# Optimization experiments

Hardware: AMD Instinct MI355X
Metric: run time of the kernel (lower is better)

## Reference

```python
import jax, jax.numpy as jnp
import numpy as np

H = 32; W = 32; KH = 3; KW = 3; NH = 8; DIM = 256; MLP_DIM = 1024; B = 4; T_FULL = 9
DH = DIM // NH
NEG = -1e9


def layernorm(x, g, b):
    m = jnp.mean(x, axis=-1, keepdims=True)
    v = jnp.var(x, axis=-1, keepdims=True)
    return (x - m) / jnp.sqrt(v + 1e-5) * g + b


def rope(x):
    # x: (B, NH, T, DH); split-half rotary position embedding
    T, dh = x.shape[-2], x.shape[-1]
    inv = 1.0 / (10000.0 ** (jnp.arange(0, dh, 2, dtype=jnp.float32) / dh))
    ang = jnp.arange(T, dtype=jnp.float32)[:, None] * inv  # (T, dh/2)
    cos, sin = jnp.cos(ang), jnp.sin(ang)
    x1, x2 = jnp.split(x, 2, axis=-1)
    return jnp.concatenate([x1 * cos - x2 * sin, x1 * sin + x2 * cos], axis=-1)


def setup_inputs() -> dict:
    key = jax.random.key(0)
    ks = jax.random.split(key, 16)
    def w(i, shp):
        return jax.random.normal(ks[i], shp, jnp.float32) * 0.02
    d = {
        'query': jax.random.normal(ks[0], (B, T_FULL, H * W, DIM), jnp.float32),
        'spatial_mask': jnp.zeros((1,), bool),          # unused by forward (module builds its own)
        'temporal_mask': jnp.zeros((T_FULL, T_FULL), bool),
        'sln_g': jnp.ones((DIM,), jnp.float32), 'sln_b': jnp.zeros((DIM,), jnp.float32),
        's_wq': w(1, (DIM, DIM)), 's_bq': jnp.zeros((DIM,), jnp.float32),
        's_wk': w(2, (DIM, DIM)), 's_bk': jnp.zeros((DIM,), jnp.float32),
        's_wv': w(3, (DIM, DIM)), 's_bv': jnp.zeros((DIM,), jnp.float32),
        's_wo': w(4, (DIM, DIM)), 's_bo': jnp.zeros((DIM,), jnp.float32),
        'tln_g': jnp.ones((DIM,), jnp.float32), 'tln_b': jnp.zeros((DIM,), jnp.float32),
        't_wq': w(5, (DIM, DIM)), 't_bq': jnp.zeros((DIM,), jnp.float32),
        't_wk': w(6, (DIM, DIM)), 't_bk': jnp.zeros((DIM,), jnp.float32),
        't_wv': w(7, (DIM, DIM)), 't_bv': jnp.zeros((DIM,), jnp.float32),
        't_wo': w(8, (DIM, DIM)), 't_bo': jnp.zeros((DIM,), jnp.float32),
        'mln_g': jnp.ones((DIM,), jnp.float32), 'mln_b': jnp.zeros((DIM,), jnp.float32),
        'w1': w(9, (DIM, MLP_DIM)), 'b1': jnp.zeros((MLP_DIM,), jnp.float32),
        'w2': w(10, (MLP_DIM, DIM)), 'b2': jnp.zeros((DIM,), jnp.float32),
    }
    return d


def _forward(query, temporal_mask, sln_g, sln_b, s_wq, s_bq, s_wk, s_bk, s_wv, s_bv, s_wo, s_bo,
             tln_g, tln_b, t_wq, t_bq, t_wk, t_bk, t_wv, t_bv, t_wo, t_bo,
             mln_g, mln_b, w1, b1, w2, b2):
    Bq, Tq, HWn, Dn = query.shape
    T = Tq - 1
    size = KH * KW
    scale = 1.0 / jnp.sqrt(jnp.float32(DH))

    # ---- spatial windowed attention on frames [:-1] (unfold -> per-window 1x9 attention) ----
    visual = query[:, :T].reshape(Bq * T, H, W, Dn)
    pad = jnp.pad(visual, ((0, 0), (KH // 2, KH // 2), (KW // 2, KW // 2), (0, 0)))
    neigh = jnp.stack([pad[:, i:i + H, j:j + W, :] for i in range(KH) for j in range(KW)], axis=1)
    neigh = neigh.reshape(Bq * T, size, HWn, Dn).transpose(0, 2, 1, 3)  # (BT, HW, size, D)
    onep = jnp.pad(jnp.ones((H, W), jnp.float32), ((KH // 2, KH // 2), (KW // 2, KW // 2)))
    valid = jnp.stack([onep[i:i + H, j:j + W] for i in range(KH) for j in range(KW)], axis=0)
    pad_mask = (valid.reshape(size, HWn).T == 0)  # (HW, size) True where neighbor from padding

    vis = visual.reshape(Bq * T, HWn, 1, Dn)
    vis_n = layernorm(vis, sln_g, sln_b)
    nei_n = layernorm(neigh, sln_g, sln_b)
    q = (vis_n @ s_wq + s_bq).reshape(Bq * T, HWn, 1, NH, DH)
    k = (nei_n @ s_wk + s_bk).reshape(Bq * T, HWn, size, NH, DH)
    v = (nei_n @ s_wv + s_bv).reshape(Bq * T, HWn, size, NH, DH)
    scores = jnp.einsum('bnqhd,bnkhd->bnhqk', q, k) * scale
    scores = jnp.where(pad_mask[None, :, None, None, :], NEG, scores)
    attn = jax.nn.softmax(scores, axis=-1)
    o = jnp.einsum('bnhqk,bnkhd->bnqhd', attn, v).reshape(Bq * T, HWn, 1, Dn)
    o = o @ s_wo + s_bo
    x_sp = (o + vis).reshape(Bq, T, HWn, Dn)

    x = jnp.concatenate([x_sp, query[:, -1:]], axis=1)  # (B, T_, HW, D)

    # ---- temporal RoPE attention per spatial location ----
    xt = x.transpose(0, 2, 1, 3).reshape(Bq * HWn, Tq, Dn)
    xn = layernorm(xt, tln_g, tln_b)
    qt = rope((xn @ t_wq + t_bq).reshape(-1, Tq, NH, DH).transpose(0, 2, 1, 3))
    kt = rope((xn @ t_wk + t_bk).reshape(-1, Tq, NH, DH).transpose(0, 2, 1, 3))
    vt = (xn @ t_wv + t_bv).reshape(-1, Tq, NH, DH).transpose(0, 2, 1, 3)
    sc = jnp.einsum('bhqd,bhkd->bhqk', qt, kt) * scale
    sc = jnp.where(temporal_mask[None, None, :, :], NEG, sc)
    at = jax.nn.softmax(sc, axis=-1)
    ot = jnp.einsum('bhqk,bhkd->bhqd', at, vt).transpose(0, 2, 1, 3).reshape(-1, Tq, Dn)
    xt = (ot @ t_wo + t_bo) + xt
    x = xt.reshape(Bq, HWn, Tq, Dn).transpose(0, 2, 1, 3)

    # CLS frame (t=0): average over spatial positions, broadcast back
    avg_cls = jnp.mean(x[:, 0], axis=1, keepdims=True)  # (B, 1, D)
    x = x.at[:, 0].set(jnp.broadcast_to(avg_cls, (Bq, HWn, Dn)))

    # ---- MLP block ----
    xm = layernorm(x, mln_g, mln_b)
    xm = jax.nn.gelu(xm @ w1 + b1, approximate=False) @ w2 + b2
    return xm + x


def reference(query, spatial_mask, temporal_mask, sln_g, sln_b, s_wq, s_bq, s_wk, s_bk, s_wv, s_bv, s_wo, s_bo, tln_g, tln_b, t_wq, t_bq, t_wk, t_bk, t_wv, t_bv, t_wo, t_bo, mln_g, mln_b, w1, b1, w2, b2):
    # spatial_mask is accepted but unused by the original forward (it rebuilds its own)
    return _forward(query, temporal_mask, sln_g, sln_b, s_wq, s_bq, s_wk, s_bk, s_wv, s_bv, s_wo, s_bo,
                    tln_g, tln_b, t_wq, t_bq, t_wk, t_bk, t_wv, t_bv, t_wo, t_bo,
                    mln_g, mln_b, w1, b1, w2, b2)
```

## Files before the change

kernel.cpp:

```cpp
#include <hip/hip_runtime.h>
#include <math.h>

#define TQ_  9

typedef unsigned int   u32;
typedef unsigned short ushort_t;
typedef short bf16x8 __attribute__((ext_vector_type(8)));
typedef float f32x4  __attribute__((ext_vector_type(4)));

__device__ __forceinline__ float bs2f(ushort_t s) {
  return __uint_as_float(((u32)s) << 16);
}
__device__ __forceinline__ ushort_t f2bs(float x) {
  u32 u = __float_as_uint(x);
  u32 r = (u + 0x7FFFu + ((u >> 16) & 1u)) >> 16;
  return (ushort_t)r;
}

__device__ __forceinline__ float gelu_f(float x) {
  float z = x * 0.70710678118654752f;
  float a = fabsf(z);
  float t = __builtin_amdgcn_rcpf(1.f + 0.3275911f * a);
  float poly = t * (0.254829592f + t * (-0.284496736f +
               t * (1.421413741f + t * (-1.453152027f + t * 1.061405429f))));
  float erfv = 1.f - poly * __expf(-z * z);
  erfv = (z < 0.f) ? -erfv : erfv;
  return 0.5f * x * (1.f + erfv);
}

struct TPA { const float* s[10]; ushort_t* d[10]; int K[10]; int N[10]; int pm[10]; };

__global__ __launch_bounds__(256)
void pack_all_kernel(TPA p) {
  int z = blockIdx.z;
  int K = p.K[z], N = p.N[z];
  int bn = blockIdx.x << 5, bk = blockIdx.y << 5;
  if (bn >= N || bk >= K) return;
  const float* W = p.s[z];
  ushort_t* pk = p.d[z];
  int pm = p.pm[z];
  __shared__ float t[32][33];
  int tid = threadIdx.x;
  int tx = tid & 31, ty = tid >> 5;
  #pragma unroll
  for (int r = 0; r < 4; ++r)
    t[ty + (r << 3)][tx] = W[(long)(bk + ty + (r << 3)) * N + bn + tx];
  __syncthreads();
  if (tid < 128) {
    int jl = tid >> 6, q = (tid >> 4) & 3, ln = tid & 15;
    int j = (bn >> 4) + jl, kk = bk >> 5;
    int colsrc = pm ? ((ln & 7) + (jl << 3) + ((ln & 8) << 1))
                    : ((jl << 4) + ln);
    long G = (((long)j * (K >> 5) + kk) << 6) + (q << 4) + ln;
    bf16x8 ov;
    #pragma unroll
    for (int e = 0; e < 8; ++e)
      ov[e] = (short)f2bs(t[(q << 3) + e][colsrc]);
    *(bf16x8*)(pk + (G << 3)) = ov;
  }
}

struct BC6 { const float* b[6]; };
__global__ __launch_bounds__(768)
void bias_concat_kernel(BC6 p, float* __restrict__ dst) {
  int z = blockIdx.x, n = threadIdx.x;
  int w = n >> 8, q = n & 255;
  int psrc = q;
  if (w < 2)
    psrc = (q & 0xE0) | (q & 7) | (((q >> 4) & 1) << 3) | (((q >> 3) & 1) << 4);
  dst[z * 768 + n] = p.b[z * 3 + w][psrc];
}

__global__ __launch_bounds__(256)
void ln_norm_kernel(const float* __restrict__ src, int spatial,
                    const float* __restrict__ g, const float* __restrict__ b,
                    ushort_t* __restrict__ dst) {
  int row = blockIdx.x * 4 + (threadIdx.x >> 6);
  int lane = threadIdx.x & 63;
  long srow = row;
  if (spatial) {
    int bq = row >> 13, r = row & 8191;
    srow = ((long)(bq * TQ_ + (r >> 10)) << 10) + (r & 1023);
  }
  float4 v = ((const float4*)(src + srow * 256))[lane];
  float s  = v.x + v.y + v.z + v.w;
  float s2 = v.x * v.x + v.y * v.y + v.z * v.z + v.w * v.w;
  #pragma unroll
  for (int m = 32; m; m >>= 1) {
    s  += __shfl_xor(s,  m, 64);
    s2 += __shfl_xor(s2, m, 64);
  }
  float mean = s * (1.f / 256.f);
  float rstd = rsqrtf(s2 * (1.f / 256.f) - mean * mean + 1e-5f);
  float4 gv = ((const float4*)g)[lane];
  float4 bv = ((const float4*)b)[lane];
  ushort_t o[4];
  o[0] = f2bs((v.x - mean) * rstd * gv.x + bv.x);
  o[1] = f2bs((v.y - mean) * rstd * gv.y + bv.y);
  o[2] = f2bs((v.z - mean) * rstd * gv.z + bv.z);
  o[3] = f2bs((v.w - mean) * rstd * gv.w + bv.w);
  u32 lo = (u32)o[0] | ((u32)o[1] << 16);
  u32 hi = (u32)o[2] | ((u32)o[3] << 16);
  uint2 pk; pk.x = lo; pk.y = hi;
  *(uint2*)(dst + (long)row * 256 + lane * 4) = pk;
}

template<int K>
__global__ __launch_bounds__(256, 4)
void wgemm_kernel(const ushort_t* __restrict__ A, int lda,
                  const ushort_t* __restrict__ packW,
                  const float* __restrict__ bias, const float* __restrict__ resid,
                  float* __restrict__ Cf, ushort_t* __restrict__ Cb,
                  int N, int NBq, int resid_mode, int out_mode, int act, int rope) {
  constexpr int K32 = K / 32;
  constexpr int AD = (K32 >= 4) ? 4 : K32;
  constexpr int BD = 2;

  int tid = threadIdx.x;
  int wv = tid >> 6, lane = tid & 63;
  int ln = lane & 15, q4 = lane >> 4;

  int gid = blockIdx.x;
  int g = gid >> 5, r = gid & 31;
  int nq = (r >> 3) + ((g % NBq) << 2);
  int mb = ((g / NBq) << 3) + (r & 7);
  int m0 = mb << 7, n0 = nq << 6;

  const ushort_t* Ap = A + (long)(m0 + (wv << 5) + ln) * lda + (q4 << 3);
  long a16 = (long)lda << 4;
  const ushort_t* Bp = packW + (((long)(nq << 2) * K32) << 9) + (lane << 3);

  bf16x8 xr[AD][2];
  bf16x8 wr[BD][4];
  #pragma unroll
  for (int d = 0; d < BD; ++d)
    #pragma unroll
    for (int j = 0; j < 4; ++j)
      wr[d][j] = *(const bf16x8*)(Bp + (((long)j * K32 + d) << 9));
  #pragma unroll
  for (int d = 0; d < AD; ++d) {
    xr[d][0] = *(const bf16x8*)(Ap + d * 32);
    xr[d][1] = *(const bf16x8*)(Ap + a16 + d * 32);
  }

  f32x4 acc[2][4];
  #pragma unroll
  for (int i = 0; i < 2; ++i)
    #pragma unroll
    for (int j = 0; j < 4; ++j) acc[i][j] = 0.f;

  #pragma unroll
  for (int kk = 0; kk < K32; ++kk) {
    #pragma unroll
    for (int i = 0; i < 2; ++i)
      #pragma unroll
      for (int j = 0; j < 4; ++j)
        acc[i][j] = __builtin_amdgcn_mfma_f32_16x16x32_bf16(
            wr[kk % BD][j], xr[kk % AD][i], acc[i][j], 0, 0, 0);
    if (kk + AD < K32) {
      xr[kk % AD][0] = *(const bf16x8*)(Ap + (kk + AD) * 32);
      xr[kk % AD][1] = *(const bf16x8*)(Ap + a16 + (kk + AD) * 32);
    }
    if (kk + BD < K32) {
      #pragma unroll
      for (int j = 0; j < 4; ++j)
        wr[kk % BD][j] = *(const bf16x8*)(Bp + (((long)j * K32 + kk + BD) << 9));
    }
    __builtin_amdgcn_sched_barrier(0);
  }

  float4 bj[4];
  #pragma unroll
  for (int j = 0; j < 4; ++j)
    bj[j] = *(const float4*)(bias + n0 + (j << 4) + (q4 << 2));

  float cs_c[2][4], cs_s[2][4];
  if (rope) {
    int t = (m0 >> 10) % TQ_;
    #pragma unroll
    for (int p = 0; p < 2; ++p)
      #pragma unroll
      for (int r2 = 0; r2 < 4; ++r2) {
        float d = (float)(((q4 & 1) << 2) + r2 + (p << 3));
        float ang = (float)t * exp2f(d * -0.8304820237218406f);
        cs_c[p][r2] = cosf(ang);
        float s = sinf(ang);
        cs_s[p][r2] = (q4 & 2) ? s : -s;
      }
  }

  #pragma unroll
  for (int i = 0; i < 2; ++i) {
    int m = m0 + (wv << 5) + (i << 4) + ln;
    long orow = m;
    if (out_mode == 1 || resid_mode == 2) {
      int bq = m >> 13, rr = m & 8191;
      orow = ((long)(bq * TQ_ + (rr >> 10)) << 10) + (rr & 1023);
    }
    #pragma unroll
    for (int j = 0; j < 4; ++j) {
      int n = n0 + (j << 4) + (q4 << 2);
      float v[4];
      #pragma unroll
      for (int r2 = 0; r2 < 4; ++r2) v[r2] = acc[i][j][r2] + bj[j][r2];
      if (rope && ((nq << 2) + j) < 32) {
        #pragma unroll
        for (int r2 = 0; r2 < 4; ++r2) {
          float other = __shfl_xor(v[r2], 32, 64);
          v[r2] = v[r2] * cs_c[j & 1][r2] + other * cs_s[j & 1][r2];
        }
      }
      if (act) {
        #pragma unroll
        for (int r2 = 0; r2 < 4; ++r2) v[r2] = gelu_f(v[r2]);
      }
      if (resid_mode == 1) {
        float4 rv = *(const float4*)(resid + (long)m * 256 + n);
        v[0] += rv.x; v[1] += rv.y; v[2] += rv.z; v[3] += rv.w;
      } else if (resid_mode == 2) {
        float4 rv = *(const float4*)(resid + orow * 256 + n);
        v[0] += rv.x; v[1] += rv.y; v[2] += rv.z; v[3] += rv.w;
      }
      if (out_mode == 2) {
        uint2 pk;
        pk.x = (u32)f2bs(v[0]) | ((u32)f2bs(v[1]) << 16);
        pk.y = (u32)f2bs(v[2]) | ((u32)f2bs(v[3]) << 16);
        *(uint2*)(Cb + (long)m * N + n) = pk;
      } else {
        float4 o4; o4.x = v[0]; o4.y = v[1]; o4.z = v[2]; o4.w = v[3];
        if (out_mode == 1) *(float4*)(Cf + orow * 256 + n) = o4;
        else               *(float4*)(Cf + (long)m * N + n) = o4;
      }
    }
  }
}

__device__ __forceinline__ int tl_off(int row, int col) {
  return (row << 8) + (((((col >> 3) + row) & 31)) << 3) + (col & 7);
}

__global__ __launch_bounds__(512, 6)
void mlp_fused_kernel(float* xio,
                      const ushort_t* __restrict__ W1p,
                      const float* __restrict__ b1,
                      const ushort_t* __restrict__ W2p,
                      const float* __restrict__ b2,
                      const float* __restrict__ g,
                      const float* __restrict__ be) {
  __shared__ ushort_t XL[8192];
  __shared__ ushort_t HLDS[8192];
  int tid = threadIdx.x;
  int wv = tid >> 6, lane = tid & 63;
  int ln = lane & 15, q4 = lane >> 4;
  int m0 = blockIdx.x << 5;

  {
    int lrow = (wv << 2) + (lane >> 4);
    int p = lane & 15;
    const float* xr = xio + (long)(m0 + lrow) * 256 + (p << 2);
    float s = 0.f, s2 = 0.f;
    float4 vbuf[4];
    #pragma unroll
    for (int k = 0; k < 4; ++k) {
      float4 a = *(const float4*)(xr + (k << 6));
      vbuf[k] = a;
      s  += a.x + a.y + a.z + a.w;
      s2 += a.x*a.x + a.y*a.y + a.z*a.z + a.w*a.w;
    }
    s  += __shfl_xor(s,  1, 64);  s  += __shfl_xor(s,  2, 64);
    s  += __shfl_xor(s,  4, 64);  s  += __shfl_xor(s,  8, 64);
    s2 += __shfl_xor(s2, 1, 64);  s2 += __shfl_xor(s2, 2, 64);
    s2 += __shfl_xor(s2, 4, 64);  s2 += __shfl_xor(s2, 8, 64);
    float mean = s * (1.f / 256.f);
    float rstd = rsqrtf(s2 * (1.f / 256.f) - mean * mean + 1e-5f);
    #pragma unroll
    for (int k = 0; k < 4; ++k) {
      int col = (p << 2) + (k << 6);
      float4 gv = *(const float4*)(g + col);
      float4 bv = *(const float4*)(be + col);
      float4 a = vbuf[k];
      u32 lo = (u32)f2bs((a.x - mean) * rstd * gv.x + bv.x)
             | ((u32)f2bs((a.y - mean) * rstd * gv.y + bv.y) << 16);
      u32 hi = (u32)f2bs((a.z - mean) * rstd * gv.z + bv.z)
             | ((u32)f2bs((a.w - mean) * rstd * gv.w + bv.w) << 16);
      uint2 pk; pk.x = lo; pk.y = hi;
      *(uint2*)&XL[tl_off(lrow, col)] = pk;
    }
  }
  __syncthreads();

  f32x4 acc[2][2];
  #pragma unroll
  for (int i = 0; i < 2; ++i)
    #pragma unroll
    for (int jl = 0; jl < 2; ++jl) acc[i][jl] = 0.f;

  #pragma unroll 1
  for (int q = 0; q < 4; ++q) {
    {
      int c32 = (q << 3) + wv;
      f32x4 h[2][2];
      #pragma unroll
      for (int i = 0; i < 2; ++i)
        #pragma unroll
        for (int jj = 0; jj < 2; ++jj) h[i][jj] = 0.f;

      bf16x8 wf[2][2];
      #pragma unroll
      for (int jj = 0; jj < 2; ++jj)
        wf[0][jj] = *(const bf16x8*)(W1p +
            (((long)((c32 << 1) + jj) * 8) << 9) + (lane << 3));
      #pragma unroll
      for (int ks = 0; ks < 8; ++ks) {
        if (ks + 1 < 8) {
          #pragma unroll
          for (int jj = 0; jj < 2; ++jj)
            wf[(ks + 1) & 1][jj] = *(const bf16x8*)(W1p +
                (((long)((c32 << 1) + jj) * 8 + ks + 1) << 9) + (lane << 3));
        }
        int col = (q4 << 3) + (ks << 5);
        bf16x8 xf0 = *(const bf16x8*)&XL[tl_off(ln, col)];
        bf16x8 xf1 = *(const bf16x8*)&XL[tl_off(16 + ln, col)];
        #pragma unroll
        for (int jj = 0; jj < 2; ++jj) {
          h[0][jj] = __builtin_amdgcn_mfma_f32_16x16x32_bf16(
              wf[ks & 1][jj], xf0, h[0][jj], 0, 0, 0);
          h[1][jj] = __builtin_amdgcn_mfma_f32_16x16x32_bf16(
              wf[ks & 1][jj], xf1, h[1][jj], 0, 0, 0);
        }
        __builtin_amdgcn_sched_barrier(0);
      }
      #pragma unroll
      for (int jj = 0; jj < 2; ++jj) {
        float4 b1v = *(const float4*)(b1 + (c32 << 5) + (jj << 4) + (q4 << 2));
        #pragma unroll
        for (int i = 0; i < 2; ++i) {
          float v[4];
          v[0] = gelu_f(h[i][jj][0] + b1v.x);
          v[1] = gelu_f(h[i][jj][1] + b1v.y);
          v[2] = gelu_f(h[i][jj][2] + b1v.z);
          v[3] = gelu_f(h[i][jj][3] + b1v.w);
          uint2 pk;
          pk.x = (u32)f2bs(v[0]) | ((u32)f2bs(v[1]) << 16);
          pk.y = (u32)f2bs(v[2]) | ((u32)f2bs(v[3]) << 16);
          *(uint2*)&HLDS[tl_off((i << 4) + ln, (wv << 5) + (jj << 4) + (q4 << 2))] = pk;
        }
      }
    }
    __syncthreads();

    {
      bf16x8 wf2[2][2];
      #pragma unroll
      for (int jl = 0; jl < 2; ++jl)
        wf2[0][jl] = *(const bf16x8*)(W2p +
            (((long)((wv << 1) + jl) * 32 + (q << 3)) << 9) + (lane << 3));
      #pragma unroll
      for (int kc = 0; kc < 8; ++kc) {
        if (kc + 1 < 8) {
          #pragma unroll
          for (int jl = 0; jl < 2; ++jl)
            wf2[(kc + 1) & 1][jl] = *(const bf16x8*)(W2p +
                (((long)((wv << 1) + jl) * 32 + (q << 3) + kc + 1) << 9) + (lane << 3));
        }
        int col = (kc << 5) + (q4 << 3);
        bf16x8 hb0 = *(const bf16x8*)&HLDS[tl_off(ln, col)];
        bf16x8 hb1 = *(const bf16x8*)&HLDS[tl_off(16 + ln, col)];
        #pragma unroll
        for (int jl = 0; jl < 2; ++jl) {
          acc[0][jl] = __builtin_amdgcn_mfma_f32_16x16x32_bf16(
              wf2[kc & 1][jl], hb0, acc[0][jl], 0, 0, 0);
          acc[1][jl] = __builtin_amdgcn_mfma_f32_16x16x32_bf16(
              wf2[kc & 1][jl], hb1, acc[1][jl], 0, 0, 0);
        }
        __builtin_amdgcn_sched_barrier(0);
      }
    }
    __syncthreads();
  }

  #pragma unroll
  for (int i = 0; i < 2; ++i) {
    long ro = (long)(m0 + (i << 4) + ln) * 256;
    #pragma unroll
    for (int jl = 0; jl < 2; ++jl) {
      int n = ((wv << 1) + jl) * 16 + (q4 << 2);
      float4 rv = *(const float4*)(xio + ro + n);
      float4 bv = *(const float4*)(b2 + n);
      float4 o;
      o.x = acc[i][jl][0] + bv.x + rv.x;
      o.y = acc[i][jl][1] + bv.y + rv.y;
      o.z = acc[i][jl][2] + bv.z + rv.z;
      o.w = acc[i][jl][3] + bv.w + rv.w;
      *(float4*)(xio + ro + n) = o;
    }
  }
}

__global__ __launch_bounds__(256)
void spatial_attn_kernel(ushort_t* __restrict__ qkv) {
  int gid = blockIdx.x * 256 + threadIdx.x;
  int head = gid & 7, pixel = gid >> 3;
  int pix = pixel & 1023, bt = pixel >> 10;
  int y = pix >> 5, x = pix & 31;
  long rb = (long)bt << 10;
  const float scale = 0.17677669529663687f;

  float qf[32];
  long qoff = (long)pixel * 768 + head * 32;
  #pragma unroll
  for (int i = 0; i < 4; ++i) {
    bf16x8 t = *(const bf16x8*)(qkv + qoff + i * 8);
    #pragma unroll
    for (int e = 0; e < 8; ++e) qf[i * 8 + e] = bs2f((ushort_t)t[e]);
  }

  float s[9];
  bool val[9];
  #pragma unroll
  for (int n = 0; n < 9; ++n) {
    int yy = y + n / 3 - 1, xx = x + n % 3 - 1;
    bool ok = ((unsigned)yy < 32u) & ((unsigned)xx < 32u);
    val[n] = ok;
    float d = 0.f;
    if (ok) {
      long ko = (rb + (yy << 5) + xx) * 768 + 256 + head * 32;
      #pragma unroll
      for (int i = 0; i < 4; ++i) {
        bf16x8 t = *(const bf16x8*)(qkv + ko + i * 8);
        #pragma unroll
        for (int e = 0; e < 8; ++e) d += qf[i * 8 + e] * bs2f((ushort_t)t[e]);
      }
    }
    s[n] = d * scale;
  }
  float mx = -1e30f;
  #pragma unroll
  for (int n = 0; n < 9; ++n) if (val[n]) mx = fmaxf(mx, s[n]);
  float sum = 0.f;
  #pragma unroll
  for (int n = 0; n < 9; ++n) { s[n] = val[n] ? __expf(s[n] - mx) : 0.f; sum += s[n]; }
  float inv = 1.f / sum;

  float o[32];
  #pragma unroll
  for (int i = 0; i < 32; ++i) o[i] = 0.f;
  #pragma unroll
  for (int n = 0; n < 9; ++n) {
    if (val[n]) {
      int yy = y + n / 3 - 1, xx = x + n % 3 - 1;
      long vo = (rb + (yy << 5) + xx) * 768 + 512 + head * 32;
      #pragma unroll
      for (int i = 0; i < 4; ++i) {
        bf16x8 t = *(const bf16x8*)(qkv + vo + i * 8);
        #pragma unroll
        for (int e = 0; e < 8; ++e) o[i * 8 + e] += s[n] * bs2f((ushort_t)t[e]);
      }
    }
  }
  #pragma unroll
  for (int i = 0; i < 4; ++i) {
    bf16x8 t;
    #pragma unroll
    for (int e = 0; e < 8; ++e) t[e] = (short)f2bs(o[i * 8 + e] * inv);
    *(bf16x8*)(qkv + qoff + i * 8) = t;
  }
}

__global__ __launch_bounds__(256)
void temporal_attn_kernel(ushort_t* __restrict__ qkv) {
  int tid = threadIdx.x;
  int head = tid & 7, hwi = tid >> 3;
  int bi = blockIdx.x;
  int tq = bi >> 7;
  int rest = bi & 127;
  int b = rest >> 5, hwg = rest & 31;
  int hw = (hwg << 5) + hwi;
  long base = (long)(b * TQ_) * 1024 + hw;
  const float scale = 0.17677669529663687f;

  float qf[32];
  long qoff = (base + (long)tq * 1024) * 768 + head * 32;
  #pragma unroll
  for (int i = 0; i < 4; ++i) {
    bf16x8 t = *(const bf16x8*)(qkv + qoff + i * 8);
    #pragma unroll
    for (int e = 0; e < 8; ++e) qf[i * 8 + e] = bs2f((ushort_t)t[e]);
  }
  float s[9];
  #pragma unroll
  for (int tk = 0; tk < 9; ++tk) {
    long ko = (base + (long)tk * 1024) * 768 + 256 + head * 32;
    float d = 0.f;
    #pragma unroll
    for (int i = 0; i < 4; ++i) {
      bf16x8 t = *(const bf16x8*)(qkv + ko + i * 8);
      #pragma unroll
      for (int e = 0; e < 8; ++e) d += qf[i * 8 + e] * bs2f((ushort_t)t[e]);
    }
    s[tk] = d * scale;
  }
  float mx = s[0];
  #pragma unroll
  for (int tk = 1; tk < 9; ++tk) mx = fmaxf(mx, s[tk]);
  float sum = 0.f;
  #pragma unroll
  for (int tk = 0; tk < 9; ++tk) { s[tk] = __expf(s[tk] - mx); sum += s[tk]; }
  float inv = 1.f / sum;

  float o[32];
  #pragma unroll
  for (int i = 0; i < 32; ++i) o[i] = 0.f;
  #pragma unroll
  for (int tk = 0; tk < 9; ++tk) {
    long vo = (base + (long)tk * 1024) * 768 + 512 + head * 32;
    #pragma unroll
    for (int i = 0; i < 4; ++i) {
      bf16x8 t = *(const bf16x8*)(qkv + vo + i * 8);
      #pragma unroll
      for (int e = 0; e < 8; ++e) o[i * 8 + e] += s[tk] * bs2f((ushort_t)t[e]);
    }
  }
  #pragma unroll
  for (int i = 0; i < 4; ++i) {
    bf16x8 t;
    #pragma unroll
    for (int e = 0; e < 8; ++e) t[e] = (short)f2bs(o[i * 8 + e] * inv);
    *(bf16x8*)(qkv + qoff + i * 8) = t;
  }
}

__global__ __launch_bounds__(256)
void copy_frame8_kernel(const float* __restrict__ qy, float* __restrict__ x) {
  long i = (long)blockIdx.x * 256 + threadIdx.x;
  int b = (int)(i >> 18);
  long rem = i & ((1L << 18) - 1);
  long gi = ((long)(b * TQ_ + 8) << 18) + rem;
  x[gi] = qy[gi];
}

__global__ __launch_bounds__(256)
void cls_sum_kernel(const float* __restrict__ x, float* __restrict__ partial) {
  int b = blockIdx.x >> 5, ch = blockIdx.x & 31;
  int d = threadIdx.x;
  long base = ((long)(b * TQ_) * 1024 + ch * 32) * 256 + d;
  float s = 0.f;
  for (int r = 0; r < 32; ++r) s += x[base + (long)r * 256];
  partial[(long)blockIdx.x * 256 + d] = s;
}

__global__ __launch_bounds__(256)
void cls_bcast_kernel(float* __restrict__ x, const float* __restrict__ partial) {
  int b = blockIdx.x >> 3, seg = blockIdx.x & 7;
  int d = threadIdx.x;
  float s = 0.f;
  for (int j = 0; j < 32; ++j) s += partial[(long)(b * 32 + j) * 256 + d];
  s *= (1.f / 1024.f);
  long base = ((long)(b * TQ_) * 1024 + seg * 128) * 256 + d;
  for (int r = 0; r < 128; ++r) x[base + (long)r * 256] = s;
}

extern "C" void kernel_launch(void* const* d_in, const int* in_sizes, int n_in,
                              void* d_out, int out_size, void* d_ws, size_t ws_size,
                              hipStream_t stream) {
  (void)in_sizes; (void)n_in; (void)out_size; (void)ws_size;
  const float* query = (const float*)d_in[0];
  const float* sln_g = (const float*)d_in[3];
  const float* sln_b = (const float*)d_in[4];
  const float* s_wq  = (const float*)d_in[5];
  const float* s_bq  = (const float*)d_in[6];
  const float* s_wk  = (const float*)d_in[7];
  const float* s_bk  = (const float*)d_in[8];
  const float* s_wv  = (const float*)d_in[9];
  const float* s_bv  = (const float*)d_in[10];
  const float* s_wo  = (const float*)d_in[11];
  const float* s_bo  = (const float*)d_in[12];
  const float* tln_g = (const float*)d_in[13];
  const float* tln_b = (const float*)d_in[14];
  const float* t_wq  = (const float*)d_in[15];
  const float* t_bq  = (const float*)d_in[16];
  const float* t_wk  = (const float*)d_in[17];
  const float* t_bk  = (const float*)d_in[18];
  const float* t_wv  = (const float*)d_in[19];
  const float* t_bv  = (const float*)d_in[20];
  const float* t_wo  = (const float*)d_in[21];
  const float* t_bo  = (const float*)d_in[22];
  const float* mln_g = (const float*)d_in[23];
  const float* mln_b = (const float*)d_in[24];
  const float* w1    = (const float*)d_in[25];
  const float* b1    = (const float*)d_in[26];
  const float* w2    = (const float*)d_in[27];
  const float* b2    = (const float*)d_in[28];
  float* out = (float*)d_out;

  const long RB = 36864L * 256;
  ushort_t* XA  = (ushort_t*)d_ws;
  ushort_t* QKV = XA + RB;
  float*    P4  = (float*)(QKV + 3 * RB);
  ushort_t* wt  = (ushort_t*)(P4 + RB);
  float* bias2  = (float*)(wt + 1048576);
  float* clsp   = bias2 + 1536;

  ushort_t* pk_sqkv = wt;
  ushort_t* pk_tqkv = wt + 196608;
  ushort_t* pk_swo  = wt + 393216;
  ushort_t* pk_two  = wt + 458752;
  ushort_t* pk_w1   = wt + 524288;
  ushort_t* pk_w2   = wt + 786432;

  TPA tp;
  tp.s[0] = s_wq; tp.d[0] = pk_sqkv;          tp.K[0] = 256;  tp.N[0] = 256;  tp.pm[0] = 1;
  tp.s[1] = s_wk; tp.d[1] = pk_sqkv + 65536;  tp.K[1] = 256;  tp.N[1] = 256;  tp.pm[1] = 1;
  tp.s[2] = s_wv; tp.d[2] = pk_sqkv + 131072; tp.K[2] = 256;  tp.N[2] = 256;  tp.pm[2] = 0;
  tp.s[3] = t_wq; tp.d[3] = pk_tqkv;          tp.K[3] = 256;  tp.N[3] = 256;  tp.pm[3] = 1;
  tp.s[4] = t_wk; tp.d[4] = pk_tqkv + 65536;  tp.K[4] = 256;  tp.N[4] = 256;  tp.pm[4] = 1;
  tp.s[5] = t_wv; tp.d[5] = pk_tqkv + 131072; tp.K[5] = 256;  tp.N[5] = 256;  tp.pm[5] = 0;
  tp.s[6] = s_wo; tp.d[6] = pk_swo;           tp.K[6] = 256;  tp.N[6] = 256;  tp.pm[6] = 0;
  tp.s[7] = t_wo; tp.d[7] = pk_two;           tp.K[7] = 256;  tp.N[7] = 256;  tp.pm[7] = 0;
  tp.s[8] = w1;   tp.d[8] = pk_w1;            tp.K[8] = 256;  tp.N[8] = 1024; tp.pm[8] = 0;
  tp.s[9] = w2;   tp.d[9] = pk_w2;            tp.K[9] = 1024; tp.N[9] = 256;  tp.pm[9] = 0;
  pack_all_kernel<<<dim3(32, 32, 10), 256, 0, stream>>>(tp);
  BC6 bc;
  bc.b[0] = s_bq; bc.b[1] = s_bk; bc.b[2] = s_bv;
  bc.b[3] = t_bq; bc.b[4] = t_bk; bc.b[5] = t_bv;
  bias_concat_kernel<<<2, 768, 0, stream>>>(bc, bias2);

  #define WGEMM(KV, Ap, ldav, Wp, bi, rs, CF, CB, M, N, rm, om, ac, rp)     \
    wgemm_kernel<KV><<<dim3(((M) / 128) * ((N) / 64)), 256, 0, stream>>>(   \
        Ap, ldav, Wp, bi, rs, CF, CB, N, (N) / 256, rm, om, ac, rp)

  ln_norm_kernel<<<8192, 256, 0, stream>>>(query, 1, sln_g, sln_b, XA);
  WGEMM(256, XA, 256, pk_sqkv, bias2, nullptr, nullptr, QKV,
        32768, 768, 0, 2, 0, 0);
  spatial_attn_kernel<<<1024, 256, 0, stream>>>(QKV);
  WGEMM(256, QKV, 768, pk_swo, s_bo, query, P4, nullptr,
        32768, 256, 2, 1, 0, 0);
  copy_frame8_kernel<<<4096, 256, 0, stream>>>(query, P4);

  ln_norm_kernel<<<9216, 256, 0, stream>>>(P4, 0, tln_g, tln_b, XA);
  WGEMM(256, XA, 256, pk_tqkv, bias2 + 768, nullptr, nullptr, QKV,
        36864, 768, 0, 2, 0, 1);
  temporal_attn_kernel<<<1152, 256, 0, stream>>>(QKV);
  WGEMM(256, QKV, 768, pk_two, t_bo, P4, out, nullptr,
        36864, 256, 1, 0, 0, 0);

  cls_sum_kernel<<<128, 256, 0, stream>>>(out, clsp);
  cls_bcast_kernel<<<32, 256, 0, stream>>>(out, clsp);

  mlp_fused_kernel<<<1152, 512, 0, stream>>>(out, pk_w1, b1, pk_w2, b2,
                                             mln_g, mln_b);
  #undef WGEMM
}
```

Baseline: 482.3 us.

## Fuse frame-8 copy and CLS broadcast into consumers, widen MLP hidden chunks, tanh GELU

Drops the frame-8 copy kernel: the temporal LayerNorm and the output-projection residual now read frame 8 directly from the query via an alternate pointer. Drops the CLS broadcast kernel: the fused MLP kernel reduces the per-batch partial sums itself and uses the average as both its input and its residual for t=0 blocks. The MLP hidden dimension is now processed in two 512-wide chunks instead of four 256-wide ones, which doubles the hidden LDS buffer and may lower occupancy. The exact erf GELU is replaced with the cheaper tanh approximation, which adds a small numerical deviation from the reference.

```diff
diff --git a/kernel.cpp b/kernel.cpp
--- a/kernel.cpp
+++ b/kernel.cpp
@@ -18,14 +18,10 @@
 }
 
 __device__ __forceinline__ float gelu_f(float x) {
-  float z = x * 0.70710678118654752f;
-  float a = fabsf(z);
-  float t = __builtin_amdgcn_rcpf(1.f + 0.3275911f * a);
-  float poly = t * (0.254829592f + t * (-0.284496736f +
-               t * (1.421413741f + t * (-1.453152027f + t * 1.061405429f))));
-  float erfv = 1.f - poly * __expf(-z * z);
-  erfv = (z < 0.f) ? -erfv : erfv;
-  return 0.5f * x * (1.f + erfv);
+  float u = 0.7978845608f * x * (1.f + 0.044715f * x * x);
+  float e = __expf(2.f * u);
+  float t = 1.f - 2.f * __builtin_amdgcn_rcpf(e + 1.f);
+  return 0.5f * x * (1.f + t);
 }
 
 struct TPA { const float* s[10]; ushort_t* d[10]; int K[10]; int N[10]; int pm[10]; };
@@ -72,17 +68,21 @@
 }
 
 __global__ __launch_bounds__(256)
-void ln_norm_kernel(const float* __restrict__ src, int spatial,
+void ln_norm_kernel(const float* __restrict__ src, const float* __restrict__ alt,
+                    int spatial,
                     const float* __restrict__ g, const float* __restrict__ b,
                     ushort_t* __restrict__ dst) {
   int row = blockIdx.x * 4 + (threadIdx.x >> 6);
   int lane = threadIdx.x & 63;
   long srow = row;
+  const float* sp = src;
   if (spatial) {
     int bq = row >> 13, r = row & 8191;
     srow = ((long)(bq * TQ_ + (r >> 10)) << 10) + (r & 1023);
-  }
-  float4 v = ((const float4*)(src + srow * 256))[lane];
+  } else if (alt && ((row >> 10) % TQ_) == 8) {
+    sp = alt;
+  }
+  float4 v = ((const float4*)(sp + srow * 256))[lane];
   float s  = v.x + v.y + v.z + v.w;
   float s2 = v.x * v.x + v.y * v.y + v.z * v.z + v.w * v.w;
   #pragma unroll
@@ -110,6 +110,7 @@
 void wgemm_kernel(const ushort_t* __restrict__ A, int lda,
                   const ushort_t* __restrict__ packW,
                   const float* __restrict__ bias, const float* __restrict__ resid,
+                  const float* __restrict__ resid2,
                   float* __restrict__ Cf, ushort_t* __restrict__ Cb,
                   int N, int NBq, int resid_mode, int out_mode, int act, int rope) {
   constexpr int K32 = K / 32;
@@ -125,6 +126,13 @@
   int nq = (r >> 3) + ((g % NBq) << 2);
   int mb = ((g / NBq) << 3) + (r & 7);
   int m0 = mb << 7, n0 = nq << 6;
+
+  const float* resid_eff = resid;
+  int rm = resid_mode;
+  if (rm == 3) {
+    if (((m0 >> 10) % TQ_) == 8) resid_eff = resid2;
+    rm = 1;
+  }
 
   const ushort_t* Ap = A + (long)(m0 + (wv << 5) + ln) * lda + (q4 << 3);
   long a16 = (long)lda << 4;
@@ -193,7 +201,7 @@
   for (int i = 0; i < 2; ++i) {
     int m = m0 + (wv << 5) + (i << 4) + ln;
     long orow = m;
-    if (out_mode == 1 || resid_mode == 2) {
+    if (out_mode == 1 || rm == 2) {
       int bq = m >> 13, rr = m & 8191;
       orow = ((long)(bq * TQ_ + (rr >> 10)) << 10) + (rr & 1023);
     }
@@ -214,11 +222,11 @@
         #pragma unroll
         for (int r2 = 0; r2 < 4; ++r2) v[r2] = gelu_f(v[r2]);
       }
-      if (resid_mode == 1) {
-        float4 rv = *(const float4*)(resid + (long)m * 256 + n);
+      if (rm == 1) {
+        float4 rv = *(const float4*)(resid_eff + (long)m * 256 + n);
         v[0] += rv.x; v[1] += rv.y; v[2] += rv.z; v[3] += rv.w;
-      } else if (resid_mode == 2) {
-        float4 rv = *(const float4*)(resid + orow * 256 + n);
+      } else if (rm == 2) {
+        float4 rv = *(const float4*)(resid_eff + orow * 256 + n);
         v[0] += rv.x; v[1] += rv.y; v[2] += rv.z; v[3] += rv.w;
       }
       if (out_mode == 2) {
@@ -238,9 +246,13 @@
 __device__ __forceinline__ int tl_off(int row, int col) {
   return (row << 8) + (((((col >> 3) + row) & 31)) << 3) + (col & 7);
 }
+__device__ __forceinline__ int t5_off(int row, int col) {
+  return (row << 9) + (((((col >> 3) + row) & 63)) << 3) + (col & 7);
+}
 
 __global__ __launch_bounds__(512, 6)
 void mlp_fused_kernel(float* xio,
+                      const float* __restrict__ clsp,
                       const ushort_t* __restrict__ W1p,
                       const float* __restrict__ b1,
                       const ushort_t* __restrict__ W2p,
@@ -248,11 +260,23 @@
                       const float* __restrict__ g,
                       const float* __restrict__ be) {
   __shared__ ushort_t XL[8192];
-  __shared__ ushort_t HLDS[8192];
+  __shared__ ushort_t HLDS[16384];
+  __shared__ float AVGL[256];
   int tid = threadIdx.x;
   int wv = tid >> 6, lane = tid & 63;
   int ln = lane & 15, q4 = lane >> 4;
   int m0 = blockIdx.x << 5;
+  int t0blk = ((m0 >> 10) % TQ_) == 0;
+  int bidx = m0 / (TQ_ * 1024);
+
+  if (t0blk && tid < 256) {
+    float s = 0.f;
+    #pragma unroll 4
+    for (int j = 0; j < 32; ++j)
+      s += clsp[(long)(bidx * 32 + j) * 256 + tid];
+    AVGL[tid] = s * (1.f / 1024.f);
+  }
+  __syncthreads();
 
   {
     int lrow = (wv << 2) + (lane >> 4);
@@ -262,7 +286,8 @@
     float4 vbuf[4];
     #pragma unroll
     for (int k = 0; k < 4; ++k) {
-      float4 a = *(const float4*)(xr + (k << 6));
+      float4 a = t0blk ? *(const float4*)&AVGL[(p << 2) + (k << 6)]
+                       : *(const float4*)(xr + (k << 6));
       vbuf[k] = a;
       s  += a.x + a.y + a.z + a.w;
       s2 += a.x*a.x + a.y*a.y + a.z*a.z + a.w*a.w;
@@ -296,54 +321,54 @@
     for (int jl = 0; jl < 2; ++jl) acc[i][jl] = 0.f;
 
   #pragma unroll 1
-  for (int q = 0; q < 4; ++q) {
+  for (int h = 0; h < 2; ++h) {
     {
-      int c32 = (q << 3) + wv;
-      f32x4 h[2][2];
+      int c = (h << 3) + wv;
+      f32x4 hh[2][4];
       #pragma unroll
       for (int i = 0; i < 2; ++i)
         #pragma unroll
-        for (int jj = 0; jj < 2; ++jj) h[i][jj] = 0.f;
-
-      bf16x8 wf[2][2];
-      #pragma unroll
-      for (int jj = 0; jj < 2; ++jj)
+        for (int jj = 0; jj < 4; ++jj) hh[i][jj] = 0.f;
+
+      bf16x8 wf[2][4];
+      #pragma unroll
+      for (int jj = 0; jj < 4; ++jj)
         wf[0][jj] = *(const bf16x8*)(W1p +
-            (((long)((c32 << 1) + jj) * 8) << 9) + (lane << 3));
+            (((long)((c << 2) + jj) * 8) << 9) + (lane << 3));
       #pragma unroll
       for (int ks = 0; ks < 8; ++ks) {
         if (ks + 1 < 8) {
           #pragma unroll
-          for (int jj = 0; jj < 2; ++jj)
+          for (int jj = 0; jj < 4; ++jj)
             wf[(ks + 1) & 1][jj] = *(const bf16x8*)(W1p +
-                (((long)((c32 << 1) + jj) * 8 + ks + 1) << 9) + (lane << 3));
+                (((long)((c << 2) + jj) * 8 + ks + 1) << 9) + (lane << 3));
         }
         int col = (q4 << 3) + (ks << 5);
         bf16x8 xf0 = *(const bf16x8*)&XL[tl_off(ln, col)];
         bf16x8 xf1 = *(const bf16x8*)&XL[tl_off(16 + ln, col)];
         #pragma unroll
-        for (int jj = 0; jj < 2; ++jj) {
-          h[0][jj] = __builtin_amdgcn_mfma_f32_16x16x32_bf16(
-              wf[ks & 1][jj], xf0, h[0][jj], 0, 0, 0);
-          h[1][jj] = __builtin_amdgcn_mfma_f32_16x16x32_bf16(
-              wf[ks & 1][jj], xf1, h[1][jj], 0, 0, 0);
+        for (int jj = 0; jj < 4; ++jj) {
+          hh[0][jj] = __builtin_amdgcn_mfma_f32_16x16x32_bf16(
+              wf[ks & 1][jj], xf0, hh[0][jj], 0, 0, 0);
+          hh[1][jj] = __builtin_amdgcn_mfma_f32_16x16x32_bf16(
+              wf[ks & 1][jj], xf1, hh[1][jj], 0, 0, 0);
         }
         __builtin_amdgcn_sched_barrier(0);
       }
       #pragma unroll
-      for (int jj = 0; jj < 2; ++jj) {
-        float4 b1v = *(const float4*)(b1 + (c32 << 5) + (jj << 4) + (q4 << 2));
+      for (int jj = 0; jj < 4; ++jj) {
+        float4 b1v = *(const float4*)(b1 + (c << 6) + (jj << 4) + (q4 << 2));
         #pragma unroll
         for (int i = 0; i < 2; ++i) {
           float v[4];
-          v[0] = gelu_f(h[i][jj][0] + b1v.x);
-          v[1] = gelu_f(h[i][jj][1] + b1v.y);
-          v[2] = gelu_f(h[i][jj][2] + b1v.z);
-          v[3] = gelu_f(h[i][jj][3] + b1v.w);
+          v[0] = gelu_f(hh[i][jj][0] + b1v.x);
+          v[1] = gelu_f(hh[i][jj][1] + b1v.y);
+          v[2] = gelu_f(hh[i][jj][2] + b1v.z);
+          v[3] = gelu_f(hh[i][jj][3] + b1v.w);
           uint2 pk;
           pk.x = (u32)f2bs(v[0]) | ((u32)f2bs(v[1]) << 16);
           pk.y = (u32)f2bs(v[2]) | ((u32)f2bs(v[3]) << 16);
-          *(uint2*)&HLDS[tl_off((i << 4) + ln, (wv << 5) + (jj << 4) + (q4 << 2))] = pk;
+          *(uint2*)&HLDS[t5_off((i << 4) + ln, (wv << 6) + (jj << 4) + (q4 << 2))] = pk;
         }
       }
     }
@@ -354,18 +379,18 @@
       #pragma unroll
       for (int jl = 0; jl < 2; ++jl)
         wf2[0][jl] = *(const bf16x8*)(W2p +
-            (((long)((wv << 1) + jl) * 32 + (q << 3)) << 9) + (lane << 3));
-      #pragma unroll
-      for (int kc = 0; kc < 8; ++kc) {
-        if (kc + 1 < 8) {
+            (((long)((wv << 1) + jl) * 32 + (h << 4)) << 9) + (lane << 3));
+      #pragma unroll
+      for (int kc = 0; kc < 16; ++kc) {
+        if (kc + 1 < 16) {
           #pragma unroll
           for (int jl = 0; jl < 2; ++jl)
             wf2[(kc + 1) & 1][jl] = *(const bf16x8*)(W2p +
-                (((long)((wv << 1) + jl) * 32 + (q << 3) + kc + 1) << 9) + (lane << 3));
+                (((long)((wv << 1) + jl) * 32 + (h << 4) + kc + 1) << 9) + (lane << 3));
         }
         int col = (kc << 5) + (q4 << 3);
-        bf16x8 hb0 = *(const bf16x8*)&HLDS[tl_off(ln, col)];
-        bf16x8 hb1 = *(const bf16x8*)&HLDS[tl_off(16 + ln, col)];
+        bf16x8 hb0 = *(const bf16x8*)&HLDS[t5_off(ln, col)];
+        bf16x8 hb1 = *(const bf16x8*)&HLDS[t5_off(16 + ln, col)];
         #pragma unroll
         for (int jl = 0; jl < 2; ++jl) {
           acc[0][jl] = __builtin_amdgcn_mfma_f32_16x16x32_bf16(
@@ -385,7 +410,8 @@
     #pragma unroll
     for (int jl = 0; jl < 2; ++jl) {
       int n = ((wv << 1) + jl) * 16 + (q4 << 2);
-      float4 rv = *(const float4*)(xio + ro + n);
+      float4 rv = t0blk ? *(const float4*)&AVGL[n]
+                        : *(const float4*)(xio + ro + n);
       float4 bv = *(const float4*)(b2 + n);
       float4 o;
       o.x = acc[i][jl][0] + bv.x + rv.x;
@@ -531,15 +557,6 @@
 }
 
 __global__ __launch_bounds__(256)
-void copy_frame8_kernel(const float* __restrict__ qy, float* __restrict__ x) {
-  long i = (long)blockIdx.x * 256 + threadIdx.x;
-  int b = (int)(i >> 18);
-  long rem = i & ((1L << 18) - 1);
-  long gi = ((long)(b * TQ_ + 8) << 18) + rem;
-  x[gi] = qy[gi];
-}
-
-__global__ __launch_bounds__(256)
 void cls_sum_kernel(const float* __restrict__ x, float* __restrict__ partial) {
   int b = blockIdx.x >> 5, ch = blockIdx.x & 31;
   int d = threadIdx.x;
@@ -547,17 +564,6 @@
   float s = 0.f;
   for (int r = 0; r < 32; ++r) s += x[base + (long)r * 256];
   partial[(long)blockIdx.x * 256 + d] = s;
-}
-
-__global__ __launch_bounds__(256)
-void cls_bcast_kernel(float* __restrict__ x, const float* __restrict__ partial) {
-  int b = blockIdx.x >> 3, seg = blockIdx.x & 7;
-  int d = threadIdx.x;
-  float s = 0.f;
-  for (int j = 0; j < 32; ++j) s += partial[(long)(b * 32 + j) * 256 + d];
-  s *= (1.f / 1024.f);
-  long base = ((long)(b * TQ_) * 1024 + seg * 128) * 256 + d;
-  for (int r = 0; r < 128; ++r) x[base + (long)r * 256] = s;
 }
 
 extern "C" void kernel_launch(void* const* d_in, const int* in_sizes, int n_in,
@@ -625,29 +631,27 @@
   bc.b[3] = t_bq; bc.b[4] = t_bk; bc.b[5] = t_bv;
   bias_concat_kernel<<<2, 768, 0, stream>>>(bc, bias2);
 
-  #define WGEMM(KV, Ap, ldav, Wp, bi, rs, CF, CB, M, N, rm, om, ac, rp)     \
-    wgemm_kernel<KV><<<dim3(((M) / 128) * ((N) / 64)), 256, 0, stream>>>(   \
-        Ap, ldav, Wp, bi, rs, CF, CB, N, (N) / 256, rm, om, ac, rp)
-
-  ln_norm_kernel<<<8192, 256, 0, stream>>>(query, 1, sln_g, sln_b, XA);
-  WGEMM(256, XA, 256, pk_sqkv, bias2, nullptr, nullptr, QKV,
+  #define WGEMM(KV, Ap, ldav, Wp, bi, rs, rs2, CF, CB, M, N, rm, om, ac, rp) \
+    wgemm_kernel<KV><<<dim3(((M) / 128) * ((N) / 64)), 256, 0, stream>>>(    \
+        Ap, ldav, Wp, bi, rs, rs2, CF, CB, N, (N) / 256, rm, om, ac, rp)
+
+  ln_norm_kernel<<<8192, 256, 0, stream>>>(query, nullptr, 1, sln_g, sln_b, XA);
+  WGEMM(256, XA, 256, pk_sqkv, bias2, nullptr, nullptr, nullptr, QKV,
         32768, 768, 0, 2, 0, 0);
   spatial_attn_kernel<<<1024, 256, 0, stream>>>(QKV);
-  WGEMM(256, QKV, 768, pk_swo, s_bo, query, P4, nullptr,
+  WGEMM(256, QKV, 768, pk_swo, s_bo, query, nullptr, P4, nullptr,
         32768, 256, 2, 1, 0, 0);
-  copy_frame8_kernel<<<4096, 256, 0, stream>>>(query, P4);
-
-  ln_norm_kernel<<<9216, 256, 0, stream>>>(P4, 0, tln_g, tln_b, XA);
-  WGEMM(256, XA, 256, pk_tqkv, bias2 + 768, nullptr, nullptr, QKV,
+
+  ln_norm_kernel<<<9216, 256, 0, stream>>>(P4, query, 0, tln_g, tln_b, XA);
+  WGEMM(256, XA, 256, pk_tqkv, bias2 + 768, nullptr, nullptr, nullptr, QKV,
         36864, 768, 0, 2, 0, 1);
   temporal_attn_kernel<<<1152, 256, 0, stream>>>(QKV);
-  WGEMM(256, QKV, 768, pk_two, t_bo, P4, out, nullptr,
-        36864, 256, 1, 0, 0, 0);
+  WGEMM(256, QKV, 768, pk_two, t_bo, P4, query, out, nullptr,
+        36864, 256, 3, 0, 0, 0);
 
   cls_sum_kernel<<<128, 256, 0, stream>>>(out, clsp);
-  cls_bcast_kernel<<<32, 256, 0, stream>>>(out, clsp);
-
-  mlp_fused_kernel<<<1152, 512, 0, stream>>>(out, pk_w1, b1, pk_w2, b2,
+
+  mlp_fused_kernel<<<1152, 512, 0, stream>>>(out, clsp, pk_w1, b1, pk_w2, b2,
                                              mln_g, mln_b);
   #undef WGEMM
 }
```

New measurement: 540.1 us. +12.0%, slower.
